# Optimization experiments

Hardware: AMD Instinct MI355X
Metric: run time of the kernel (lower is better)

## Reference

```python
import jax, jax.numpy as jnp
import numpy as np

MAX_DISP = 48
B, C, H, W = 2, 32, 128, 240


def setup_inputs() -> dict:
    key = jax.random.key(0)
    k1, k2 = jax.random.split(key)
    l_fmap = jax.random.normal(k1, (B, C, H, W), dtype=jnp.float32)
    r_fmap = jax.random.normal(k2, (B, C, H, W), dtype=jnp.float32)
    return {"l_fmap": l_fmap, "r_fmap": r_fmap}


def reference(l_fmap, r_fmap):
    # Output: [B, C, D, H, W] where out[..., d, :, w] =
    #   l[..., w] - r[..., w-d]  if w >= d else 1.0 (pad value)
    D = MAX_DISP
    Wdim = l_fmap.shape[-1]
    w = jnp.arange(Wdim)                       # [W]
    d = jnp.arange(D)[:, None]                 # [D,1]
    shift_idx = jnp.maximum(w[None, :] - d, 0) # [D,W], clamped gather index
    # Gather shifted right features: [B,C,H,W] indexed on last axis by [D,W] -> [B,C,H,D,W]
    r_shifted = r_fmap[..., shift_idx]
    r_shifted = jnp.transpose(r_shifted, (0, 1, 3, 2, 4))  # [B,C,D,H,W]
    diff = l_fmap[:, :, None, :, :] - r_shifted            # [B,C,D,H,W]
    valid = (w[None, :] >= d)                              # [D,W]
    cost_volume = jnp.where(valid[None, None, :, None, :], diff,
                            jnp.float32(1.0))
    return cost_volume
```

## Files before the change

### kernel.cpp

```cpp
#include <hip/hip_runtime.h>


#define MAX_DISP 48
#define HH 128
#define WW 240

__global__ __launch_bounds__(256) void costvol_kernel(
    const float* __restrict__ l,
    const float* __restrict__ r,
    float* __restrict__ out)
{
    __shared__ float r_row[WW];

    const int bch = blockIdx.x;
    const int h   = bch % HH;
    const int bc  = bch / HH;
    const int tid = threadIdx.x;

    const size_t base_in = (size_t)bch * WW;

    float lval = 0.0f;
    if (tid < WW) {
        r_row[tid] = r[base_in + tid];
        lval       = l[base_in + tid];
    }
    __syncthreads();

    if (tid >= WW) return;
    const int w = tid;

    size_t obase = ((size_t)bc * MAX_DISP * HH + (size_t)h) * WW + (size_t)w;
    const size_t dstride = (size_t)HH * WW;

    #pragma unroll
    for (int d = 0; d < MAX_DISP; ++d) {
        int idx = w - d;
        float rv = r_row[idx < 0 ? 0 : idx];
        float v  = (w >= d) ? (lval - rv) : 1.0f;
        out[obase + (size_t)d * dstride] = v;
    }
}

extern "C" void kernel_launch(void* const* d_in, const int* in_sizes, int n_in,
                              void* d_out, int out_size, void* d_ws, size_t ws_size,
                              hipStream_t stream) {
    const float* l = (const float*)d_in[0];
    const float* r = (const float*)d_in[1];
    float* out = (float*)d_out;

    const int nblocks = 2 * 32 * HH;
    costvol_kernel<<<nblocks, 256, 0, stream>>>(l, r, out);
}
```

Measured before the change: 94.58 us.

## Vectorize cost volume stores to float4 with padded shared row and nontemporal writes

Each thread now handles four adjacent width positions and writes float4 outputs. The four wavefronts of a block split the disparities among themselves. The right feature row is zero-padded in shared memory so shifted float4 reads need no clamping, and out-of-range lanes are selected from two aligned vectors. Stores use nontemporal hints to avoid polluting cache on the large write-only output. The aim is fewer, wider store instructions on a store-bandwidth-bound kernel, at the cost of more select logic and 4 idle lanes per wave.

New measurement: 77.59 us (median of 2 runs). -18.0%, faster.

```diff
diff --git a/kernel.cpp b/kernel.cpp
--- a/kernel.cpp
+++ b/kernel.cpp
@@ -4,50 +4,69 @@
 #define MAX_DISP 48
 #define HH 128
 #define WW 240
+#define NV 60
+#define PAD4 12
+
+typedef float f32x4 __attribute__((ext_vector_type(4)));
 
 __global__ __launch_bounds__(256) void costvol_kernel(
-    const float* __restrict__ l,
+    const f32x4* __restrict__ l4,
     const float* __restrict__ r,
-    float* __restrict__ out)
+    f32x4* __restrict__ out4)
 {
-    __shared__ float r_row[WW];
+    __shared__ float r_pad[48 + WW];
 
     const int bch = blockIdx.x;
     const int h   = bch % HH;
     const int bc  = bch / HH;
     const int tid = threadIdx.x;
+    const int v   = tid & 63;
+    const int kg  = tid >> 6;
 
-    const size_t base_in = (size_t)bch * WW;
+    if (tid < 48)  r_pad[tid] = 0.0f;
+    if (tid < WW)  r_pad[48 + tid] = r[(size_t)bch * WW + tid];
 
-    float lval = 0.0f;
-    if (tid < WW) {
-        r_row[tid] = r[base_in + tid];
-        lval       = l[base_in + tid];
-    }
+    f32x4 lv = {0.f, 0.f, 0.f, 0.f};
+    if (v < NV) lv = l4[(size_t)bch * NV + v];
     __syncthreads();
 
-    if (tid >= WW) return;
-    const int w = tid;
+    if (v >= NV) return;
 
-    size_t obase = ((size_t)bc * MAX_DISP * HH + (size_t)h) * WW + (size_t)w;
-    const size_t dstride = (size_t)HH * WW;
+    const f32x4* rp4 = (const f32x4*)r_pad;
+    const size_t  dstride4 = (size_t)HH * NV;
+    const int     w0 = 4 * v;
 
     #pragma unroll
-    for (int d = 0; d < MAX_DISP; ++d) {
-        int idx = w - d;
-        float rv = r_row[idx < 0 ? 0 : idx];
-        float v  = (w >= d) ? (lval - rv) : 1.0f;
-        out[obase + (size_t)d * dstride] = v;
+    for (int iter = 0; iter < 3; ++iter) {
+        const int k  = kg + 4 * iter;
+        const int d0 = 4 * k;
+
+        f32x4 A = rp4[PAD4 + v - k];
+        f32x4 B = rp4[PAD4 + v - k - 1];
+
+        size_t ob = ((size_t)(bc * MAX_DISP + d0) * HH + h) * NV + v;
+
+        #pragma unroll
+        for (int s = 0; s < 4; ++s) {
+            f32x4 o;
+            #pragma unroll
+            for (int j = 0; j < 4; ++j) {
+                const int src = j - s;
+                float rv = (src >= 0) ? A[src] : B[4 + src];
+                o[j] = (w0 + j >= d0 + s) ? (lv[j] - rv) : 1.0f;
+            }
+            __builtin_nontemporal_store(o, &out4[ob + (size_t)s * dstride4]);
+        }
     }
 }
 
 extern "C" void kernel_launch(void* const* d_in, const int* in_sizes, int n_in,
                               void* d_out, int out_size, void* d_ws, size_t ws_size,
                               hipStream_t stream) {
-    const float* l = (const float*)d_in[0];
-    const float* r = (const float*)d_in[1];
-    float* out = (float*)d_out;
+    const f32x4* l4 = (const f32x4*)d_in[0];
+    const float* r  = (const float*)d_in[1];
+    f32x4* out4 = (f32x4*)d_out;
 
     const int nblocks = 2 * 32 * HH;
-    costvol_kernel<<<nblocks, 256, 0, stream>>>(l, r, out);
+    costvol_kernel<<<nblocks, 256, 0, stream>>>(l4, r, out4);
 }
```
